# Kernel tuning notes

Measured on AMD Instinct MI355X. Metric: run time of the kernel, lower is better.

## Reference

```python
import jax, jax.numpy as jnp
import numpy as np

DIM = 512
NUM_HEADS = 8
HEAD_DIM = DIM // NUM_HEADS
SCALE = HEAD_DIM ** -0.5


def setup_inputs() -> dict:
    key = jax.random.key(0)
    ks = jax.random.split(key, 6)
    B, N = 2, 4096
    x = jax.random.normal(ks[0], (B, N, DIM), dtype=jnp.float32)
    # xavier_uniform for qkv [3*dim, dim] and proj [dim, dim] (torch Linear weight layout [out,in])
    lim_qkv = float(np.sqrt(6.0 / (3 * DIM + DIM)))
    w_qkv = jax.random.uniform(ks[1], (3 * DIM, DIM), minval=-lim_qkv, maxval=lim_qkv, dtype=jnp.float32)
    lim_p = float(np.sqrt(6.0 / (DIM + DIM)))
    w_proj = jax.random.uniform(ks[2], (DIM, DIM), minval=-lim_p, maxval=lim_p, dtype=jnp.float32)
    b_proj = jnp.zeros((DIM,), dtype=jnp.float32)
    ln_gamma = jnp.ones((DIM,), dtype=jnp.float32)
    ln_beta = jnp.zeros((DIM,), dtype=jnp.float32)
    return {"x": x, "w_qkv": w_qkv, "w_proj": w_proj, "b_proj": b_proj,
            "ln_gamma": ln_gamma, "ln_beta": ln_beta}


def _attention(x, w_qkv, w_proj, b_proj, ln_gamma, ln_beta):
    B, N, C = x.shape
    qkv = jnp.einsum('bnc,dc->bnd', x, w_qkv)              # [B,N,3C]
    qkv = qkv.reshape(B, N, 3, NUM_HEADS, HEAD_DIM)
    qkv = jnp.transpose(qkv, (2, 0, 3, 1, 4))              # [3,B,H,N,Dh]
    q, k, v = qkv[0], qkv[1], qkv[2]
    attn = jnp.einsum('bhnd,bhmd->bhnm', q, k) * SCALE     # [B,H,N,N]
    attn = jax.nn.softmax(attn, axis=-1)
    # dropout is identity in eval mode
    out = jnp.einsum('bhnm,bhmd->bhnd', attn, v)           # [B,H,N,Dh]
    out = jnp.transpose(out, (0, 2, 1, 3)).reshape(B, N, C)
    out = jnp.einsum('bnc,dc->bnd', out, w_proj) + b_proj
    y = x + out
    mean = jnp.mean(y, axis=-1, keepdims=True)
    var = jnp.var(y, axis=-1, keepdims=True)
    return (y - mean) / jnp.sqrt(var + 1e-5) * ln_gamma + ln_beta


def reference(x, w_qkv, w_proj, b_proj, ln_gamma, ln_beta):
    return _attention(x, w_qkv, w_proj, b_proj, ln_gamma, ln_beta)
```

## Files before the change

kernel.cpp:

```cpp
#include <hip/hip_runtime.h>
#include <hip/hip_bf16.h>

#define SEQ    4096
#define CDIM   512
#define NHEADS 8
#define HDIM   64
#define QSCALE 0.18033688f

typedef __attribute__((ext_vector_type(4))) float f32x4;
typedef __attribute__((ext_vector_type(8))) short bf16x8;

__device__ __forceinline__ int swz(int row, int col) {
    int b = (row << 7) + (col << 1);
    b ^= (row & 7) << 4;
    return b >> 1;
}

__device__ __forceinline__ short f2bf(float f) {
    union { __hip_bfloat16 h; short s; } u;
    u.h = __float2bfloat16(f);
    return u.s;
}

__device__ __forceinline__ void gl16(const void* g, void* l) {
    __builtin_amdgcn_global_load_lds(
        (const __attribute__((address_space(1))) unsigned int*)g,
        (__attribute__((address_space(3))) unsigned int*)l,
        16, 0, 0);
}

__global__ __launch_bounds__(256) void cvt_k(
    const float* __restrict__ a, short* __restrict__ o, int n4)
{
    int i = blockIdx.x * 256 + threadIdx.x;
    const int stride = gridDim.x * 256;
    for (; i < n4; i += stride) {
        float4 v = ((const float4*)a)[i];
        short4 r;
        r.x = f2bf(v.x); r.y = f2bf(v.y); r.z = f2bf(v.z); r.w = f2bf(v.w);
        ((short4*)o)[i] = r;
    }
}

__global__ __launch_bounds__(256) void qkv_gemm_k(
    const short* __restrict__ xb, const short* __restrict__ wb,
    short* __restrict__ qb, short* __restrict__ kb, short* __restrict__ vtb)
{
    __shared__ alignas(16) short As[2][128 * 64];
    __shared__ alignas(16) short Bs[2][128 * 64];
    const int tid  = threadIdx.x;
    const int lane = tid & 63;
    const int l15  = lane & 15;
    const int lg   = lane >> 4;
    const int wv   = tid >> 6;
    const int wy   = wv >> 1, wx = wv & 1;
    const int m0 = blockIdx.x * 128;
    const int n0 = blockIdx.y * 128;

    const f32x4 fzero = {0.f, 0.f, 0.f, 0.f};
    f32x4 acc[4][4];
    #pragma unroll
    for (int i = 0; i < 4; ++i)
        #pragma unroll
        for (int j = 0; j < 4; ++j)
            acc[i][j] = fzero;

    const int row0 = wv * 8 + (lane >> 3);
    const int cb   = ((lane & 7) ^ (lane >> 3)) << 4;
    const char* agp = (const char*)xb + (size_t)(m0 + row0) * 1024 + cb;
    const char* bgp = (const char*)wb + (size_t)(n0 + row0) * 1024 + cb;
    char* al0 = (char*)&As[0][0] + wv * 1024;
    char* al1 = (char*)&As[1][0] + wv * 1024;
    char* bl0 = (char*)&Bs[0][0] + wv * 1024;
    char* bl1 = (char*)&Bs[1][0] + wv * 1024;

    #define QSTAGE(al, bl, kofs) do {                                  \
        _Pragma("unroll")                                              \
        for (int i_ = 0; i_ < 4; ++i_) {                               \
            gl16(agp + (kofs) + i_ * 32768, (al) + i_ * 4096);         \
            gl16(bgp + (kofs) + i_ * 32768, (bl) + i_ * 4096);         \
        } } while (0)

    QSTAGE(al0, bl0, 0);

    int cur = 0;
    for (int k0 = 0; k0 < CDIM; k0 += 64) {
        asm volatile("s_waitcnt vmcnt(0)" ::: "memory");
        __syncthreads();
        if (k0 + 64 < CDIM) {
            if (cur == 0) QSTAGE(al1, bl1, (k0 + 64) * 2);
            else          QSTAGE(al0, bl0, (k0 + 64) * 2);
        }
        const short* Ac = cur ? &As[1][0] : &As[0][0];
        const short* Bc = cur ? &Bs[1][0] : &Bs[0][0];

        #pragma unroll
        for (int ks = 0; ks < 2; ++ks) {
            bf16x8 afr[4], bfr[4];
            #pragma unroll
            for (int i = 0; i < 4; ++i) {
                afr[i] = *(const bf16x8*)(&Ac[swz(wy * 64 + i * 16 + l15, ks * 32 + lg * 8)]);
                bfr[i] = *(const bf16x8*)(&Bc[swz(wx * 64 + i * 16 + l15, ks * 32 + lg * 8)]);
            }
            #pragma unroll
            for (int i = 0; i < 4; ++i)
                #pragma unroll
                for (int j = 0; j < 4; ++j)
                    acc[i][j] = __builtin_amdgcn_mfma_f32_16x16x32_bf16(afr[i], bfr[j], acc[i][j], 0, 0, 0);
        }
        cur ^= 1;
    }
    #undef QSTAGE

    #pragma unroll
    for (int j = 0; j < 4; ++j) {
        const int d = n0 + wx * 64 + j * 16 + l15;
        const int s = d >> 9;
        const int h = (d >> 6) & 7;
        const int e = d & 63;
        #pragma unroll
        for (int i = 0; i < 4; ++i) {
            #pragma unroll
            for (int r = 0; r < 4; ++r) {
                const int m  = m0 + wy * 64 + i * 16 + lg * 4 + r;
                const int bb = m >> 12;
                const int n  = m & (SEQ - 1);
                const int bh = bb * NHEADS + h;
                const float v = acc[i][j][r];
                if (s == 0) {
                    qb[(((size_t)bh * SEQ + n) << 6) + e] = f2bf(v * QSCALE);
                } else if (s == 1) {
                    kb[(((size_t)bh * SEQ + n) << 6) + e] = f2bf(v);
                } else {
                    const int c  = n & 63;
                    const int cp = (c & 0x23) | ((c & 0x0C) << 1) | ((c & 0x10) >> 2);
                    vtb[((size_t)bh << 18) + ((size_t)(n >> 6) << 12) + (e << 6) + cp] = f2bf(v);
                }
            }
        }
    }
}

__global__ __launch_bounds__(256) void attn_k(
    const short* __restrict__ qb, const short* __restrict__ kb, const short* __restrict__ vtb,
    short* __restrict__ ob)
{
    __shared__ alignas(16) short Ks[2][128 * 64];
    __shared__ alignas(16) short VTs[2][2 * 64 * 64];
    const int tid  = threadIdx.x;
    const int lane = tid & 63;
    const int l15  = lane & 15;
    const int lg   = lane >> 4;
    const int wv   = tid >> 6;
    const int lin  = blockIdx.x;
    const int bh   = lin & 15;
    const int q0   = (lin >> 4) << 7;
    const int b    = bh >> 3, h = bh & 7;
    const size_t base = (size_t)bh * SEQ * HDIM;

    bf16x8 qf[2][2];
    #pragma unroll
    for (int qi = 0; qi < 2; ++qi) {
        const short* qp = qb + base + (size_t)(q0 + wv * 32 + qi * 16 + l15) * HDIM + lg * 8;
        qf[qi][0] = *(const bf16x8*)(qp);
        qf[qi][1] = *(const bf16x8*)(qp + 32);
    }

    const f32x4 fzero = {0.f, 0.f, 0.f, 0.f};
    f32x4 acc[2][4];
    f32x4 lacc[2];
    #pragma unroll
    for (int qi = 0; qi < 2; ++qi) {
        lacc[qi] = fzero;
        #pragma unroll
        for (int di = 0; di < 4; ++di) acc[qi][di] = fzero;
    }

    bf16x8 ones;
    #pragma unroll
    for (int e = 0; e < 8; ++e) ones[e] = (short)0x3F80;

    const int t0  = wv * 256 + lane;
    const int cbs = ((t0 & 7) ^ ((t0 >> 3) & 7)) << 4;
    const char* kgp = (const char*)(kb + base) + (((t0 >> 3) << 7) + cbs);
    const char* vgp = (const char*)(vtb + ((size_t)bh << 18))
                    + (((t0 >> 9) << 13) + (((t0 >> 3) & 63) << 7) + cbs);
    char* kl0 = (char*)&Ks[0][0]  + wv * 4096;
    char* kl1 = (char*)&Ks[1][0]  + wv * 4096;
    char* vl0 = (char*)&VTs[0][0] + wv * 4096;
    char* vl1 = (char*)&VTs[1][0] + wv * 4096;

    #define STAGE(kl, vl, gofs) do {                               \
        _Pragma("unroll")                                          \
        for (int i_ = 0; i_ < 4; ++i_) {                           \
            gl16(kgp + (gofs) + i_ * 1024, (kl) + i_ * 1024);      \
            gl16(vgp + (gofs) + i_ * 1024, (vl) + i_ * 1024);      \
        } } while (0)

    STAGE(kl0, vl0, 0);

    int cur = 0;
    for (int kt = 0; kt < SEQ; kt += 128) {
        asm volatile("s_waitcnt vmcnt(0)" ::: "memory");
        __syncthreads();

        if (kt + 128 < SEQ) {
            if (cur == 0) STAGE(kl1, vl1, (kt + 128) * 128);
            else          STAGE(kl0, vl0, (kt + 128) * 128);
        }

        const short* Kc = cur ? &Ks[1][0]  : &Ks[0][0];
        const short* Vc = cur ? &VTs[1][0] : &VTs[0][0];

        f32x4 s[2][8];
        #pragma unroll
        for (int qi = 0; qi < 2; ++qi)
            #pragma unroll
            for (int ni = 0; ni < 8; ++ni) s[qi][ni] = fzero;
        __builtin_amdgcn_s_setprio(1);
        #pragma unroll
        for (int kk = 0; kk < 2; ++kk)
            #pragma unroll
            for (int ni = 0; ni < 8; ++ni) {
                bf16x8 kf = *(const bf16x8*)(&Kc[swz(ni * 16 + l15, kk * 32 + lg * 8)]);
                s[0][ni] = __builtin_amdgcn_mfma_f32_16x16x32_bf16(kf, qf[0][kk], s[0][ni], 0, 0, 0);
                s[1][ni] = __builtin_amdgcn_mfma_f32_16x16x32_bf16(kf, qf[1][kk], s[1][ni], 0, 0, 0);
            }
        __builtin_amdgcn_s_setprio(0);

        #pragma unroll
        for (int ks = 0; ks < 4; ++ks) {
            bf16x8 pa0, pa1;
            #pragma unroll
            for (int e = 0; e < 8; ++e) {
                pa0[e] = f2bf(__builtin_amdgcn_exp2f(s[0][ks * 2 + (e >> 2)][e & 3]));
                pa1[e] = f2bf(__builtin_amdgcn_exp2f(s[1][ks * 2 + (e >> 2)][e & 3]));
            }
            __builtin_amdgcn_s_setprio(1);
            lacc[0] = __builtin_amdgcn_mfma_f32_16x16x32_bf16(pa0, ones, lacc[0], 0, 0, 0);
            lacc[1] = __builtin_amdgcn_mfma_f32_16x16x32_bf16(pa1, ones, lacc[1], 0, 0, 0);
            #pragma unroll
            for (int di = 0; di < 4; ++di) {
                bf16x8 vfr = *(const bf16x8*)(&Vc[(ks >> 1) * 4096
                                               + swz(di * 16 + l15, (ks & 1) * 32 + lg * 8)]);
                acc[0][di] = __builtin_amdgcn_mfma_f32_16x16x32_bf16(pa0, vfr, acc[0][di], 0, 0, 0);
                acc[1][di] = __builtin_amdgcn_mfma_f32_16x16x32_bf16(pa1, vfr, acc[1][di], 0, 0, 0);
            }
            __builtin_amdgcn_s_setprio(0);
        }

        cur ^= 1;
    }
    #undef STAGE

    #pragma unroll
    for (int qi = 0; qi < 2; ++qi) {
        float inv[4];
        #pragma unroll
        for (int r = 0; r < 4; ++r) inv[r] = 1.0f / lacc[qi][r];
        #pragma unroll
        for (int di = 0; di < 4; ++di) {
            const int e = di * 16 + l15;
            #pragma unroll
            for (int r = 0; r < 4; ++r) {
                const int qn = q0 + wv * 32 + qi * 16 + lg * 4 + r;
                ob[((size_t)(b * SEQ + qn) << 9) + h * 64 + e] = f2bf(acc[qi][di][r] * inv[r]);
            }
        }
    }
}

__global__ __launch_bounds__(256) void proj_k(
    const short* __restrict__ ao, const short* __restrict__ wpb,
    const float* __restrict__ bp, const float* __restrict__ x,
    float* __restrict__ y)
{
    __shared__ alignas(16) short As[2][128 * 64];
    __shared__ alignas(16) short Bs[2][128 * 64];
    const int tid  = threadIdx.x;
    const int lane = tid & 63;
    const int l15  = lane & 15;
    const int lg   = lane >> 4;
    const int wv   = tid >> 6;
    const int wy   = wv >> 1, wx = wv & 1;
    const int m0 = blockIdx.x * 128;
    const int n0 = blockIdx.y * 128;

    const f32x4 fzero = {0.f, 0.f, 0.f, 0.f};
    f32x4 acc[4][4];
    #pragma unroll
    for (int i = 0; i < 4; ++i)
        #pragma unroll
        for (int j = 0; j < 4; ++j)
            acc[i][j] = fzero;

    const int row0 = wv * 8 + (lane >> 3);
    const int cb   = ((lane & 7) ^ (lane >> 3)) << 4;
    const char* agp = (const char*)ao  + (size_t)(m0 + row0) * 1024 + cb;
    const char* bgp = (const char*)wpb + (size_t)(n0 + row0) * 1024 + cb;
    char* al0 = (char*)&As[0][0] + wv * 1024;
    char* al1 = (char*)&As[1][0] + wv * 1024;
    char* bl0 = (char*)&Bs[0][0] + wv * 1024;
    char* bl1 = (char*)&Bs[1][0] + wv * 1024;

    #define PSTAGE(al, bl, kofs) do {                                  \
        _Pragma("unroll")                                              \
        for (int i_ = 0; i_ < 4; ++i_) {                               \
            gl16(agp + (kofs) + i_ * 32768, (al) + i_ * 4096);         \
            gl16(bgp + (kofs) + i_ * 32768, (bl) + i_ * 4096);         \
        } } while (0)

    PSTAGE(al0, bl0, 0);

    int cur = 0;
    for (int k0 = 0; k0 < CDIM; k0 += 64) {
        asm volatile("s_waitcnt vmcnt(0)" ::: "memory");
        __syncthreads();
        if (k0 + 64 < CDIM) {
            if (cur == 0) PSTAGE(al1, bl1, (k0 + 64) * 2);
            else          PSTAGE(al0, bl0, (k0 + 64) * 2);
        }
        const short* Ac = cur ? &As[1][0] : &As[0][0];
        const short* Bc = cur ? &Bs[1][0] : &Bs[0][0];

        #pragma unroll
        for (int ks = 0; ks < 2; ++ks) {
            bf16x8 afr[4], bfr[4];
            #pragma unroll
            for (int i = 0; i < 4; ++i) {
                afr[i] = *(const bf16x8*)(&Ac[swz(wy * 64 + i * 16 + l15, ks * 32 + lg * 8)]);
                bfr[i] = *(const bf16x8*)(&Bc[swz(wx * 64 + i * 16 + l15, ks * 32 + lg * 8)]);
            }
            #pragma unroll
            for (int i = 0; i < 4; ++i)
                #pragma unroll
                for (int j = 0; j < 4; ++j)
                    acc[i][j] = __builtin_amdgcn_mfma_f32_16x16x32_bf16(afr[i], bfr[j], acc[i][j], 0, 0, 0);
        }
        cur ^= 1;
    }
    #undef PSTAGE

    #pragma unroll
    for (int i = 0; i < 4; ++i) {
        #pragma unroll
        for (int j = 0; j < 4; ++j) {
            const int d = n0 + wx * 64 + j * 16 + l15;
            #pragma unroll
            for (int r = 0; r < 4; ++r) {
                const int m = m0 + wy * 64 + i * 16 + lg * 4 + r;
                const size_t idx = (size_t)m * CDIM + d;
                y[idx] = acc[i][j][r] + bp[d] + x[idx];
            }
        }
    }
}

__global__ __launch_bounds__(256) void ln_k(
    float* __restrict__ y, const float* __restrict__ gm, const float* __restrict__ bt)
{
    const int lane = threadIdx.x & 63;
    const int row  = blockIdx.x * 4 + (threadIdx.x >> 6);
    float* p = y + (size_t)row * CDIM;
    float4 a = *(const float4*)(p + lane * 4);
    float4 b = *(const float4*)(p + 256 + lane * 4);
    float s = a.x + a.y + a.z + a.w + b.x + b.y + b.z + b.w;
    float q = a.x * a.x + a.y * a.y + a.z * a.z + a.w * a.w
            + b.x * b.x + b.y * b.y + b.z * b.z + b.w * b.w;
    #pragma unroll
    for (int mm = 1; mm < 64; mm <<= 1) {
        s += __shfl_xor(s, mm, 64);
        q += __shfl_xor(q, mm, 64);
    }
    const float mean = s * (1.0f / CDIM);
    const float var  = q * (1.0f / CDIM) - mean * mean;
    const float inv  = rsqrtf(var + 1e-5f);
    float4 g0 = *(const float4*)(gm + lane * 4);
    float4 g1 = *(const float4*)(gm + 256 + lane * 4);
    float4 t0 = *(const float4*)(bt + lane * 4);
    float4 t1 = *(const float4*)(bt + 256 + lane * 4);
    float4 r0, r1;
    r0.x = (a.x - mean) * inv * g0.x + t0.x;
    r0.y = (a.y - mean) * inv * g0.y + t0.y;
    r0.z = (a.z - mean) * inv * g0.z + t0.z;
    r0.w = (a.w - mean) * inv * g0.w + t0.w;
    r1.x = (b.x - mean) * inv * g1.x + t1.x;
    r1.y = (b.y - mean) * inv * g1.y + t1.y;
    r1.z = (b.z - mean) * inv * g1.z + t1.z;
    r1.w = (b.w - mean) * inv * g1.w + t1.w;
    *(float4*)(p + lane * 4) = r0;
    *(float4*)(p + 256 + lane * 4) = r1;
}

extern "C" void kernel_launch(void* const* d_in, const int* in_sizes, int n_in,
                              void* d_out, int out_size, void* d_ws, size_t ws_size,
                              hipStream_t stream)
{
    const float* x      = (const float*)d_in[0];
    const float* w_qkv  = (const float*)d_in[1];
    const float* w_proj = (const float*)d_in[2];
    const float* b_proj = (const float*)d_in[3];
    const float* gamma  = (const float*)d_in[4];
    const float* beta   = (const float*)d_in[5];
    float* out = (float*)d_out;

    const size_t qkv_elems = (size_t)16 * SEQ * HDIM;
    short* qb    = (short*)d_ws;
    short* kb    = qb + qkv_elems;
    short* vtb   = kb + qkv_elems;
    short* ob    = vtb + qkv_elems;
    short* xb    = ob;
    short* wqkvb = ob + qkv_elems;
    short* wpb   = qb;

    cvt_k     <<<dim3(1024),   256, 0, stream>>>(x, xb, (2 * SEQ * CDIM) / 4);
    cvt_k     <<<dim3(256),    256, 0, stream>>>(w_qkv, wqkvb, (3 * CDIM * CDIM) / 4);
    qkv_gemm_k<<<dim3(64, 12), 256, 0, stream>>>(xb, wqkvb, qb, kb, vtb);
    attn_k    <<<dim3(512),    256, 0, stream>>>(qb, kb, vtb, ob);
    cvt_k     <<<dim3(256),    256, 0, stream>>>(w_proj, wpb, (CDIM * CDIM) / 4);
    proj_k    <<<dim3(64, 4),  256, 0, stream>>>(ob, wpb, b_proj, x, out);
    ln_k      <<<dim3(2048),   256, 0, stream>>>(out, gamma, beta);
}
```

Measured before the change: 130.9 us.

## Split attention KV range across two waves groups per block with LDS reduction

Each attention block now runs 512 threads as two groups of four waves. Each group processes half of the key/value sequence with its own double-buffered LDS tiles of 64 keys. At the end, group 1 writes its partial output and row-sum accumulators to LDS and group 0 adds them before normalising and storing. This raises the number of waves per block to improve latency hiding and MFMA occupancy. In exchange it uses more LDS per block, adds a cross-group reduction, and halves the key tile size, which means more barrier iterations per key.

```diff
diff --git a/kernel.cpp b/kernel.cpp
--- a/kernel.cpp
+++ b/kernel.cpp
@@ -141,17 +141,17 @@
     }
 }
 
-__global__ __launch_bounds__(256) void attn_k(
+__global__ __launch_bounds__(512) void attn_k(
     const short* __restrict__ qb, const short* __restrict__ kb, const short* __restrict__ vtb,
     short* __restrict__ ob)
 {
-    __shared__ alignas(16) short Ks[2][128 * 64];
-    __shared__ alignas(16) short VTs[2][2 * 64 * 64];
+    __shared__ alignas(16) char smem[65536];
     const int tid  = threadIdx.x;
     const int lane = tid & 63;
     const int l15  = lane & 15;
     const int lg   = lane >> 4;
-    const int wv   = tid >> 6;
+    const int wv   = (tid >> 6) & 3;
+    const int wg   = tid >> 8;
     const int lin  = blockIdx.x;
     const int bh   = lin & 15;
     const int q0   = (lin >> 4) << 7;
@@ -180,19 +180,20 @@
     #pragma unroll
     for (int e = 0; e < 8; ++e) ones[e] = (short)0x3F80;
 
-    const int t0  = wv * 256 + lane;
+    const int t0  = wv * 128 + lane;
     const int cbs = ((t0 & 7) ^ ((t0 >> 3) & 7)) << 4;
-    const char* kgp = (const char*)(kb + base) + (((t0 >> 3) << 7) + cbs);
-    const char* vgp = (const char*)(vtb + ((size_t)bh << 18))
-                    + (((t0 >> 9) << 13) + (((t0 >> 3) & 63) << 7) + cbs);
-    char* kl0 = (char*)&Ks[0][0]  + wv * 4096;
-    char* kl1 = (char*)&Ks[1][0]  + wv * 4096;
-    char* vl0 = (char*)&VTs[0][0] + wv * 4096;
-    char* vl1 = (char*)&VTs[1][0] + wv * 4096;
+    const int ghb = wg * 262144;
+    const char* kgp = (const char*)(kb + base) + ghb + (((t0 >> 3) << 7) + cbs);
+    const char* vgp = (const char*)(vtb + ((size_t)bh << 18)) + ghb + (((t0 >> 3) << 7) + cbs);
+    char* const gbase = smem + wg * 32768;
+    char* kl0 = gbase + wv * 2048;
+    char* kl1 = gbase + 8192  + wv * 2048;
+    char* vl0 = gbase + 16384 + wv * 2048;
+    char* vl1 = gbase + 16384 + 8192 + wv * 2048;
 
     #define STAGE(kl, vl, gofs) do {                               \
         _Pragma("unroll")                                          \
-        for (int i_ = 0; i_ < 4; ++i_) {                           \
+        for (int i_ = 0; i_ < 2; ++i_) {                           \
             gl16(kgp + (gofs) + i_ * 1024, (kl) + i_ * 1024);      \
             gl16(vgp + (gofs) + i_ * 1024, (vl) + i_ * 1024);      \
         } } while (0)
@@ -200,28 +201,28 @@
     STAGE(kl0, vl0, 0);
 
     int cur = 0;
-    for (int kt = 0; kt < SEQ; kt += 128) {
+    for (int kt = 0; kt < SEQ / 2; kt += 64) {
         asm volatile("s_waitcnt vmcnt(0)" ::: "memory");
         __syncthreads();
 
-        if (kt + 128 < SEQ) {
-            if (cur == 0) STAGE(kl1, vl1, (kt + 128) * 128);
-            else          STAGE(kl0, vl0, (kt + 128) * 128);
-        }
-
-        const short* Kc = cur ? &Ks[1][0]  : &Ks[0][0];
-        const short* Vc = cur ? &VTs[1][0] : &VTs[0][0];
-
-        f32x4 s[2][8];
+        if (kt + 64 < SEQ / 2) {
+            if (cur == 0) STAGE(kl1, vl1, (kt + 64) * 128);
+            else          STAGE(kl0, vl0, (kt + 64) * 128);
+        }
+
+        const short* Kc = (const short*)(gbase + cur * 8192);
+        const short* Vc = (const short*)(gbase + 16384 + cur * 8192);
+
+        f32x4 s[2][4];
         #pragma unroll
         for (int qi = 0; qi < 2; ++qi)
             #pragma unroll
-            for (int ni = 0; ni < 8; ++ni) s[qi][ni] = fzero;
+            for (int ni = 0; ni < 4; ++ni) s[qi][ni] = fzero;
         __builtin_amdgcn_s_setprio(1);
         #pragma unroll
         for (int kk = 0; kk < 2; ++kk)
             #pragma unroll
-            for (int ni = 0; ni < 8; ++ni) {
+            for (int ni = 0; ni < 4; ++ni) {
                 bf16x8 kf = *(const bf16x8*)(&Kc[swz(ni * 16 + l15, kk * 32 + lg * 8)]);
                 s[0][ni] = __builtin_amdgcn_mfma_f32_16x16x32_bf16(kf, qf[0][kk], s[0][ni], 0, 0, 0);
                 s[1][ni] = __builtin_amdgcn_mfma_f32_16x16x32_bf16(kf, qf[1][kk], s[1][ni], 0, 0, 0);
@@ -229,7 +230,7 @@
         __builtin_amdgcn_s_setprio(0);
 
         #pragma unroll
-        for (int ks = 0; ks < 4; ++ks) {
+        for (int ks = 0; ks < 2; ++ks) {
             bf16x8 pa0, pa1;
             #pragma unroll
             for (int e = 0; e < 8; ++e) {
@@ -241,8 +242,7 @@
             lacc[1] = __builtin_amdgcn_mfma_f32_16x16x32_bf16(pa1, ones, lacc[1], 0, 0, 0);
             #pragma unroll
             for (int di = 0; di < 4; ++di) {
-                bf16x8 vfr = *(const bf16x8*)(&Vc[(ks >> 1) * 4096
-                                               + swz(di * 16 + l15, (ks & 1) * 32 + lg * 8)]);
+                bf16x8 vfr = *(const bf16x8*)(&Vc[swz(di * 16 + l15, ks * 32 + lg * 8)]);
                 acc[0][di] = __builtin_amdgcn_mfma_f32_16x16x32_bf16(pa0, vfr, acc[0][di], 0, 0, 0);
                 acc[1][di] = __builtin_amdgcn_mfma_f32_16x16x32_bf16(pa1, vfr, acc[1][di], 0, 0, 0);
             }
@@ -253,18 +253,40 @@
     }
     #undef STAGE
 
-    #pragma unroll
-    for (int qi = 0; qi < 2; ++qi) {
-        float inv[4];
-        #pragma unroll
-        for (int r = 0; r < 4; ++r) inv[r] = 1.0f / lacc[qi][r];
-        #pragma unroll
-        for (int di = 0; di < 4; ++di) {
-            const int e = di * 16 + l15;
-            #pragma unroll
-            for (int r = 0; r < 4; ++r) {
-                const int qn = q0 + wv * 32 + qi * 16 + lg * 4 + r;
-                ob[((size_t)(b * SEQ + qn) << 9) + h * 64 + e] = f2bf(acc[qi][di][r] * inv[r]);
+    __syncthreads();
+    float* xch = (float*)smem;
+    const int xi = (wv * 64 + lane) * 44;
+    if (wg == 1) {
+        #pragma unroll
+        for (int qi = 0; qi < 2; ++qi) {
+            #pragma unroll
+            for (int di = 0; di < 4; ++di)
+                *(f32x4*)(xch + xi + qi * 16 + di * 4) = acc[qi][di];
+            *(f32x4*)(xch + xi + 32 + qi * 4) = lacc[qi];
+        }
+    }
+    __syncthreads();
+    if (wg == 0) {
+        #pragma unroll
+        for (int qi = 0; qi < 2; ++qi) {
+            #pragma unroll
+            for (int di = 0; di < 4; ++di)
+                acc[qi][di] += *(const f32x4*)(xch + xi + qi * 16 + di * 4);
+            lacc[qi] += *(const f32x4*)(xch + xi + 32 + qi * 4);
+        }
+        #pragma unroll
+        for (int qi = 0; qi < 2; ++qi) {
+            float inv[4];
+            #pragma unroll
+            for (int r = 0; r < 4; ++r) inv[r] = 1.0f / lacc[qi][r];
+            #pragma unroll
+            for (int di = 0; di < 4; ++di) {
+                const int e = di * 16 + l15;
+                #pragma unroll
+                for (int r = 0; r < 4; ++r) {
+                    const int qn = q0 + wv * 32 + qi * 16 + lg * 4 + r;
+                    ob[((size_t)(b * SEQ + qn) << 9) + h * 64 + e] = f2bf(acc[qi][di][r] * inv[r]);
+                }
             }
         }
     }
@@ -416,7 +438,7 @@
     cvt_k     <<<dim3(1024),   256, 0, stream>>>(x, xb, (2 * SEQ * CDIM) / 4);
     cvt_k     <<<dim3(256),    256, 0, stream>>>(w_qkv, wqkvb, (3 * CDIM * CDIM) / 4);
     qkv_gemm_k<<<dim3(64, 12), 256, 0, stream>>>(xb, wqkvb, qb, kb, vtb);
-    attn_k    <<<dim3(512),    256, 0, stream>>>(qb, kb, vtb, ob);
+    attn_k    <<<dim3(512),    512, 0, stream>>>(qb, kb, vtb, ob);
     cvt_k     <<<dim3(256),    256, 0, stream>>>(w_proj, wpb, (CDIM * CDIM) / 4);
     proj_k    <<<dim3(64, 4),  256, 0, stream>>>(ob, wpb, b_proj, x, out);
     ln_k      <<<dim3(2048),   256, 0, stream>>>(out, gamma, beta);
```

New measurement: 122.0 us. -6.8%, faster.
